# Kernel tuning notes

Measured on AMD Instinct MI355X. Metric: run time of the kernel, lower is better.

Reference implementation:

```python
import jax, jax.numpy as jnp
import numpy as np
from jax import lax

U = 45      # sliding window length (input_dim[1])
WH = 22     # half window, int(U/2)
L = 900     # fixed sequence length
D = 80      # doppler bins (input_dim[2])
DM = 40     # d_model


def _lin(x, w, b):
    return x @ w.T + b


def _conv(x, w, b):
    y = lax.conv_general_dilated(x, w, (1, 1), 'SAME', dimension_numbers=('NCHW', 'OIHW', 'NCHW'))
    return y + b[None, :, None, None]


def _pool(x, th, tw):
    return lax.reduce_window(x, -jnp.inf, lax.max, (1, 1, th, tw), (1, 1, th, tw), 'VALID')


def _encoder(x, cw1, cb1, cw2, cb2, cw3, cb3, cw4, cb4):
    x = _pool(jax.nn.elu(_conv(x, cw1, cb1)), 2, 2)  # 45x80 -> 22x40
    x = _pool(jax.nn.elu(_conv(x, cw2, cb2)), 2, 2)  # -> 11x20
    x = _pool(jax.nn.elu(_conv(x, cw3, cb3)), 2, 2)  # -> 5x10
    x = _pool(jax.nn.elu(_conv(x, cw4, cb4)), 1, 2)  # -> 5x5
    return x


def _forward(z, targets_onehot, dur, cw1, cb1, cw2, cb2, cw3, cb3, cw4, cb4,
             fc1w, fc1b, fc2w, fc2b, embw, embb, wq, bq, wk, bk, wv, bv,
             flw1, flb1, flw2, flb2, stw1, stb1, stw2, stb2, edw1, edb1, edw2, edb2):
    B = z.shape[0]
    # --- vectorized sliding-window extraction (replaces per-timestep loop) ---
    # In the original, real frames are always RIGHT-aligned inside the window
    # (zeros are concatenated at the front for both head and tail edges).
    i = jnp.arange(L)[:, None]
    j = jnp.arange(U)[None, :]
    end = jnp.minimum(i + WH + 1, L)           # exclusive end of real content
    idx = end - U + j                          # (L, U) source frame per slot
    valid = idx >= jnp.maximum(i - WH, 0)      # slots before real content are zero
    win = jnp.take(z, jnp.clip(idx, 0, L - 1), axis=2)          # (B, 1, L, U, D)
    win = jnp.where(valid[None, None, :, :, None], win, 0.0)
    win = win.transpose(0, 2, 1, 3, 4).reshape(B * L, 1, U, D)
    feat = _encoder(win, cw1, cb1, cw2, cb2, cw3, cb3, cw4, cb4).reshape(B, L, 400)
    # classifier_1 (dropout = identity in eval)
    z_p = _lin(jax.nn.elu(_lin(feat, fc1w, fc1b)), fc2w, fc2b)   # (B, L, 40)
    t = jnp.broadcast_to(targets_onehot[:, None, :], (B, L, targets_onehot.shape[-1]))
    z_t = jax.nn.elu(_lin(jnp.concatenate([z_p, t], axis=-1), embw, embb))  # (B, L, 40)
    # masked self-attention
    q = _lin(z_t, wq, bq)
    k = _lin(z_t, wk, bk)
    v = _lin(z_t, wv, bv)
    score = jnp.einsum('bld,bmd->blm', q, k) / jnp.sqrt(jnp.float32(DM))
    m = jnp.arange(L)[None, :] < dur[:, None]                    # (B, L)
    mask = m[:, :, None] & m[:, None, :]                         # (B, L, L)
    # original: score*mask then masked_fill(mask==0, -1e-12)
    score = jnp.where(mask, score, jnp.float32(-1e-12))
    attn = jax.nn.softmax(score, axis=-1)
    x = attn @ v + z_t

    def head(h, w1, b1, w2, b2):
        return _lin(jax.nn.elu(_lin(h, w1, b1)), w2, b2)[..., 0]

    fl = head(x, flw1, flb1, flw2, flb2)
    st = head(x, stw1, stb1, stw2, stb2)
    ed = head(x, edw1, edb1, edw2, edb2)
    return fl, st, ed


_PARAM_SHAPES = [('cw1', (4, 1, 3, 3)), ('cb1', (4,)), ('cw2', (8, 4, 3, 3)), ('cb2', (8,)),
                 ('cw3', (16, 8, 3, 3)), ('cb3', (16,)), ('cw4', (16, 16, 3, 3)), ('cb4', (16,)),
                 ('fc1w', (128, 400)), ('fc1b', (128,)), ('fc2w', (40, 128)), ('fc2b', (40,)),
                 ('embw', (40, 45)), ('embb', (40,)),
                 ('wq', (40, 40)), ('bq', (40,)), ('wk', (40, 40)), ('bk', (40,)), ('wv', (40, 40)), ('bv', (40,)),
                 ('flw1', (10, 40)), ('flb1', (10,)), ('flw2', (1, 10)), ('flb2', (1,)),
                 ('stw1', (10, 40)), ('stb1', (10,)), ('stw2', (1, 10)), ('stb2', (1,)),
                 ('edw1', (10, 40)), ('edb1', (10,)), ('edw2', (1, 10)), ('edb2', (1,))]


def setup_inputs() -> dict:
    key = jax.random.key(0)
    ks = jax.random.split(key, 64)
    B = 4
    inp = {}
    inp['z'] = jax.random.normal(ks[0], (B, 1, L, D), jnp.float32)
    inp['targets_onehot'] = jax.nn.one_hot(jax.random.randint(ks[1], (B,), 0, 5), 5, dtype=jnp.float32)
    inp['dur'] = jax.random.randint(ks[2], (B,), 1, L + 1)
    for t, (name, shp) in enumerate(_PARAM_SHAPES):
        inp[name] = jax.random.normal(ks[3 + t], shp, jnp.float32) * 0.05
    return inp


def reference(z, targets_onehot, dur, cw1, cb1, cw2, cb2, cw3, cb3, cw4, cb4,
              fc1w, fc1b, fc2w, fc2b, embw, embb, wq, bq, wk, bk, wv, bv,
              flw1, flb1, flw2, flb2, stw1, stb1, stw2, stb2, edw1, edb1, edw2, edb2):
    return _forward(z, targets_onehot, dur, cw1, cb1, cw2, cb2, cw3, cb3, cw4, cb4,
                    fc1w, fc1b, fc2w, fc2b, embw, embb, wq, bq, wk, bk, wv, bv,
                    flw1, flb1, flw2, flb2, stw1, stb1, stw2, stb2, edw1, edb1, edw2, edb2)
```

## Files before the change

kernel.cpp:

```cpp
#include <hip/hip_runtime.h>

typedef unsigned int u32;
typedef _Float16 f16;
typedef f16 f16x2 __attribute__((ext_vector_type(2)));
typedef f16 f16x4 __attribute__((ext_vector_type(4)));
typedef f16 f16x8 __attribute__((ext_vector_type(8)));
typedef float f32x4 __attribute__((ext_vector_type(4)));

#define LSEQ 900
#define BATCH 4
#define NWIN (BATCH*LSEQ)
#define NBLK NWIN
#define MT 57
#define NABLK (BATCH*MT)

__device__ __forceinline__ float eluf(float x){ return x > 0.f ? x : __expf(x) - 1.f; }
#define BC2(u) __builtin_bit_cast(f16x2, (u))
#define ZERO4H ((f16x4){(f16)0,(f16)0,(f16)0,(f16)0})
#define ZERO8H __builtin_bit_cast(f16x8, (uint4{0,0,0,0}))

#define P0U 0
#define P1U 2112
#define FEATU 3872
#define F32U 4080
#define SMTOT 4288
#define T1F 0
#define H2F 4224
#define T2F 0
#define H3F 4224
#define T3F 0
#define FEATF 7744

#define WB2A 0
#define WB2B 512
#define WB3  768
#define WB4  2304
#define WFC1 5376
#define WEND 58624
#define WPM  58624
#define WPTE (WPM + 576000)
#define WPZ  (WPTE + 576000)
#define WQH  (WPZ + 576000)
#define WKH  (WQH + 145920)
#define WVT  (WKH + 145920)
#define WF32 ((WVT + 145920)/2)

#define PREP_BLOCKS ((WEND+255)/256)
#define CONV_BLOCKS ((144000+255)/256)

__global__ __launch_bounds__(256) void prep_all(
    const float* __restrict__ z,
    const float* __restrict__ cw1, const float* __restrict__ cb1,
    const float* __restrict__ cw2, const float* __restrict__ cw3,
    const float* __restrict__ cw4, const float* __restrict__ fc1w,
    f16* __restrict__ wsF, f16* __restrict__ PM, f16* __restrict__ PTE, f16* __restrict__ PZ)
{
  const int blk = blockIdx.x;
  if (blk < PREP_BLOCKS) {
    const int g = blk*256 + threadIdx.x;
    if (g >= WEND) return;
    float val;
    if (g < 512) {
      const int l = g>>3, j = g&7;
      const int oc = l&15, c = l>>4;
      const int dr = c>>1, dc = 2*(c&1) + (j>>2), ic = j&3;
      val = (oc<8 && dc<3) ? cw2[oc*36 + ic*9 + dr*3 + dc] : 0.f;
    } else if (g < 768) {
      const int u = g-512, l = u>>2, j = u&3;
      const int oc = l&15, dc = l>>4, ic = j;
      val = (oc<8 && dc<3) ? cw2[oc*36 + ic*9 + 6 + dc] : 0.f;
    } else if (g < 2304) {
      const int u = g-768, dr = u>>9, r = u&511, l = r>>3, j = r&7;
      const int oc = l&15, dc = l>>4, ic = j;
      val = (dc<3) ? cw3[oc*72 + ic*9 + dr*3 + dc] : 0.f;
    } else if (g < 5376) {
      const int u = g-2304, v = u>>9, dr = v>>1, h = v&1;
      const int r = u&511, l = r>>3, j = r&7;
      const int oc = l&15, chunk = l>>4;
      const int dcl = chunk>>1, ic = (chunk&1)*8 + j, dc = h*2 + dcl;
      val = (dc<3) ? cw4[oc*144 + ic*9 + dr*3 + dc] : 0.f;
    } else {
      const int u = g - WFC1;
      const int j = u&7, l = (u>>3)&63, st = (u>>9)%13, nt = u/(13*512);
      const int k = st*32 + (l>>4)*8 + j, n = nt*16 + (l&15);
      val = (k<400) ? fc1w[n*400 + k] : 0.f;
    }
    wsF[g] = (f16)val;
  } else {
    const int g = (blk - PREP_BLOCKS)*256 + threadIdx.x;
    if (g >= 144000) return;
    const int cp = g % 40, fb2 = g / 40, f = fb2 % 900, b = fb2 / 900;
    if (f >= 899) return;
    const int c0 = 2*cp;
    const float* zb = z + b*72000;
    float p[4][4];
    #pragma unroll
    for (int dr = 0; dr < 4; ++dr) {
      const int r = f - 1 + dr;
      const bool rok = (r >= 0) && (r < 900);
      #pragma unroll
      for (int dc = 0; dc < 4; ++dc) {
        const int cc = c0 + dc - 1;
        p[dr][dc] = (rok && cc >= 0 && cc < 80) ? zb[r*80+cc] : 0.f;
      }
    }
    f16x4 opm, opte, opz;
    #pragma unroll
    for (int oc = 0; oc < 4; ++oc) {
      float pmv = -3.4e38f, ptev = -3.4e38f, pzv = -3.4e38f;
      #pragma unroll
      for (int col = 0; col < 2; ++col) {
        float te = cb1[oc];
        float s0 = 0.f;
        float c1n = cb1[oc];
        #pragma unroll
        for (int dc = 0; dc < 3; ++dc) {
          const float w0 = cw1[oc*9 + dc], w1 = cw1[oc*9 + 3 + dc], w2 = cw1[oc*9 + 6 + dc];
          s0  += w0 * p[0][col+dc];
          te  += w1 * p[1][col+dc] + w2 * p[2][col+dc];
          c1n += w0 * p[1][col+dc] + w1 * p[2][col+dc] + w2 * p[3][col+dc];
        }
        const float cf = te + s0;
        pmv  = fmaxf(pmv,  fmaxf(cf, c1n));
        ptev = fmaxf(ptev, fmaxf(te, c1n));
        pzv  = fmaxf(pzv,  fmaxf(te, 0.f));
      }
      opm[oc]  = (f16)eluf(pmv);
      opte[oc] = (f16)eluf(ptev);
      opz[oc]  = (f16)eluf(pzv);
    }
    *(f16x4*)(PM  + g*4) = opm;
    *(f16x4*)(PTE + g*4) = opte;
    *(f16x4*)(PZ  + g*4) = opz;
  }
}

__global__ __launch_bounds__(256,8) void encoder6(
    const f16* __restrict__ PM, const f16* __restrict__ PTE, const f16* __restrict__ PZ,
    const float* __restrict__ toh,
    const float* __restrict__ cb2, const float* __restrict__ cb3, const float* __restrict__ cb4,
    const f16* __restrict__ wsF,
    const float* __restrict__ fc1b, const float* __restrict__ fc2w, const float* __restrict__ fc2b,
    const float* __restrict__ embw, const float* __restrict__ embb,
    const float* __restrict__ wq, const float* __restrict__ bq,
    const float* __restrict__ wk, const float* __restrict__ bk,
    const float* __restrict__ wv, const float* __restrict__ bv,
    float* __restrict__ zt_g, f16* __restrict__ qh,
    f16* __restrict__ kh, f16* __restrict__ vT)
{
  __shared__ __align__(16) u32 sm[SMTOT];
  f16* smh = (f16*)sm;
  const int tid = threadIdx.x, blk = blockIdx.x;
  const int lane = tid & 63, wid = tid >> 6;
  const int b = blk/LSEQ, i0 = blk%LSEQ;

  {
    const int e45 = min(i0 + 23, LSEQ) - 45;
    const int sv  = max(i0 - 22, 0);
    const f16* PMb  = PM  + b*144000;
    const f16* PTEb = PTE + b*144000;
    const f16* PZb  = PZ  + b*144000;
    for (int s = tid; s < 440; s += 256) {
      const int pr = s/20, pcp = s%20;
      const int fa = e45 + 2*pr;
      f16x8 v = ZERO8H;
      if (fa > sv)         v = *(const f16x8*)(PMb  + (fa*40 + 2*pcp)*4);
      else if (fa == sv)   v = *(const f16x8*)(PTEb + (fa*40 + 2*pcp)*4);
      else if (fa == sv-1) v = *(const f16x8*)(PZb  + (sv*40 + 2*pcp)*4);
      f16* dst = smh + T1F + ((pr+1)*44 + 2*pcp+1)*4;
      *(f16x4*)(dst)     = __builtin_shufflevector(v, v, 0,1,2,3);
      *(f16x4*)(dst + 4) = __builtin_shufflevector(v, v, 4,5,6,7);
    }
    for (int s = tid; s < 176; s += 256) {
      int r, c;
      if (s < 44)      { r = 0;  c = s; }
      else if (s < 88) { r = 23; c = s-44; }
      else {
        const int t = s - 88;
        const int which = t / 22;
        r = (t % 22) + 1;
        c = which == 0 ? 0 : (which == 1 ? 41 : (which == 2 ? 42 : 43));
      }
      *(f16x4*)(smh + T1F + (r*44+c)*4) = ZERO4H;
    }
    if (tid < 2) ((uint4*)(sm))[FEATU/4 + 50 + tid] = (uint4){0,0,0,0};
  }
  __syncthreads();

  {
    const f16x8 B2a = *(const f16x8*)(wsF + WB2A + lane*8);
    const f16x4 B2b = *(const f16x4*)(wsF + WB2B + lane*4);
    const int oc = lane&15, chunk = lane>>4;
    const float bias2 = (oc<8) ? cb2[oc] : 0.f;
    int r2 = (wid*16 + oc)/40, c2 = (wid*16 + oc)%40;
    int rE = (wid*16 + chunk*4)/40, cE = (wid*16 + chunk*4)%40;
    for (int t = wid; t < 55; t += 4) {
      const f16* base = smh + T1F;
      const f16* pA = base + ((r2 + (chunk>>1))*44 + c2 + 2*(chunk&1))*4;
      const f16x4 lo = *(const f16x4*)(pA);
      const f16x4 hi = *(const f16x4*)(pA + 4);
      const f16x8 a8 = __builtin_shufflevector(lo, hi, 0,1,2,3,4,5,6,7);
      f32x4 acc = {bias2, bias2, bias2, bias2};
      acc = __builtin_amdgcn_mfma_f32_16x16x32_f16(a8, B2a, acc, 0, 0, 0);
      const f16x4 a4 = *(const f16x4*)(base + ((r2+2)*44 + c2 + chunk)*4);
      acc = __builtin_amdgcn_mfma_f32_16x16x16f16(a4, B2b, acc, 0, 0, 0);
      if (oc < 8) {
        f16* h2o = smh + H2F;
        h2o[(rE*20 + (cE>>1))*8 + oc] = (f16)fmaxf(acc[0], acc[1]);
        const int cE2 = cE + 2;
        const int rE2 = rE + (cE2 >= 40 ? 1 : 0);
        const int cE3 = cE2 >= 40 ? cE2 - 40 : cE2;
        h2o[(rE2*20 + (cE3>>1))*8 + oc] = (f16)fmaxf(acc[2], acc[3]);
      }
      { const int cn = c2 + 24; const int cy = cn >= 40;
        r2 += 1 + cy; c2 = cy ? cn - 40 : cn; }
      { const int cn = cE + 24; const int cy = cn >= 40;
        rE += 1 + cy; cE = cy ? cn - 40 : cn; }
    }
  }
  __syncthreads();

  {
    for (int s = tid; s < 312; s += 256) {
      const int r = s/24, c = s%24;
      if (!(r>=1 && r<=11 && c>=1 && c<=20)) {
        const uint4 z4 = {0,0,0,0};
        *(uint4*)(smh + T2F + (r*24+c)*8) = z4;
      }
    }
    for (int s = tid; s < 880; s += 256) {
      const int pr = s/80, rem = s%80, cp = rem/4, op = rem%4;
      const u32* h2 = (const u32*)(smh + H2F);
      const u32 a  = h2[((2*pr  )*20 + cp)*4 + op];
      const u32 b2 = h2[((2*pr+1)*20 + cp)*4 + op];
      const f16x2 av = BC2(a), bv = BC2(b2);
      f16x2 o;
      o.x = (f16)eluf(fmaxf((float)av.x, (float)bv.x));
      o.y = (f16)eluf(fmaxf((float)av.y, (float)bv.y));
      ((u32*)(smh + T2F))[((pr+1)*24 + cp+1)*4 + op] = __builtin_bit_cast(u32, o);
    }
  }
  __syncthreads();

  {
    f16x8 B3r[3];
    #pragma unroll
    for (int dr = 0; dr < 3; ++dr) B3r[dr] = *(const f16x8*)(wsF + WB3 + dr*512 + lane*8);
    const int oc = lane&15, chunk = lane>>4;
    const float bias3 = cb3[oc];
    for (int t = wid; t < 14; t += 4) {
      const int mA = t*16 + oc;
      const int r3 = mA/20, c3 = mA%20;
      const f16* base = smh + T2F;
      f32x4 acc = {bias3, bias3, bias3, bias3};
      #pragma unroll
      for (int dr = 0; dr < 3; ++dr) {
        const f16x8 a8 = *(const f16x8*)(base + ((r3+dr)*24 + c3 + chunk)*8);
        acc = __builtin_amdgcn_mfma_f32_16x16x32_f16(a8, B3r[dr], acc, 0, 0, 0);
      }
      #pragma unroll
      for (int p = 0; p < 2; ++p) {
        const int mE = t*16 + chunk*4 + 2*p;
        if (mE < 220) {
          const int rE = mE/20, cE = mE%20;
          if (rE < 10)
            smh[H3F + (rE*10 + (cE>>1))*16 + oc] = (f16)fmaxf(acc[2*p], acc[2*p+1]);
        }
      }
    }
  }
  __syncthreads();

  {
    for (int s = tid; s < 98; s += 256) {
      const int r = s/14, c = s%14;
      if (!(r>=1 && r<=5 && c>=1 && c<=10)) {
        const uint4 z4 = {0,0,0,0};
        *(uint4*)(smh + T3F + (r*14+c)*16)     = z4;
        *(uint4*)(smh + T3F + (r*14+c)*16 + 8) = z4;
      }
    }
    for (int s = tid; s < 400; s += 256) {
      const int pr = s/80, rem = s%80, cp = rem/8, op = rem%8;
      const u32* h3 = (const u32*)(smh + H3F);
      const u32 a  = h3[((2*pr  )*10 + cp)*8 + op];
      const u32 b2 = h3[((2*pr+1)*10 + cp)*8 + op];
      const f16x2 av = BC2(a), bv = BC2(b2);
      f16x2 o;
      o.x = (f16)eluf(fmaxf((float)av.x, (float)bv.x));
      o.y = (f16)eluf(fmaxf((float)av.y, (float)bv.y));
      ((u32*)(smh + T3F))[((pr+1)*14 + cp+1)*8 + op] = __builtin_bit_cast(u32, o);
    }
  }
  __syncthreads();

  {
    f16x8 B4r[6];
    #pragma unroll
    for (int v = 0; v < 6; ++v) B4r[v] = *(const f16x8*)(wsF + WB4 + v*512 + lane*8);
    const int oc = lane&15, chunk = lane>>4;
    const int dcl = chunk>>1, hsel = chunk&1;
    const float bias4 = cb4[oc];
    for (int t = wid; t < 4; t += 4) {
      const int mA = t*16 + oc;
      const int mmA = mA < 50 ? mA : mA - 50;
      const int r4 = mmA/10, c4 = mmA%10;
      const f16* base = smh + T3F;
      f32x4 acc = {bias4, bias4, bias4, bias4};
      #pragma unroll
      for (int v = 0; v < 6; ++v) {
        const int dr = v>>1, h = v&1;
        const f16x8 a8 = *(const f16x8*)(base + ((r4+dr)*14 + c4 + h*2 + dcl)*16 + hsel*8);
        acc = __builtin_amdgcn_mfma_f32_16x16x32_f16(a8, B4r[v], acc, 0, 0, 0);
      }
      #pragma unroll
      for (int p = 0; p < 2; ++p) {
        const int mE = t*16 + chunk*4 + 2*p;
        if (mE < 50) {
          const int rE = mE/10, cE = mE%10;
          smh[FEATF + oc*25 + rE*5 + (cE>>1)] = (f16)eluf(fmaxf(acc[2*p], acc[2*p+1]));
        }
      }
    }
  }
  __syncthreads();

  {
    float* h1 = (float*)(sm + F32U);
    #pragma unroll
    for (int q2 = 0; q2 < 2; ++q2) {
      const int nt = wid + q2*4;
      f32x4 acc = {0.f, 0.f, 0.f, 0.f};
      for (int st = 0; st < 13; ++st) {
        const f16x8 a8 = *(const f16x8*)(smh + FEATF + st*32 + (lane>>4)*8);
        const f16x8 b8 = *(const f16x8*)(wsF + WFC1 + ((nt*13 + st)*64 + lane)*8);
        acc = __builtin_amdgcn_mfma_f32_16x16x32_f16(a8, b8, acc, 0, 0, 0);
      }
      if (lane < 16) {
        const int n = nt*16 + lane;
        h1[n] = eluf(acc[0] + fc1b[n]);
      }
    }
  }
  __syncthreads();

  if (wid == 0) {
    float* h1f = (float*)(sm + F32U);
    float* zpf = h1f + 128;
    float* ztf = h1f + 168;
    if (lane < 40) {
      const float4* hv = (const float4*)h1f;
      const float4* wr = (const float4*)(fc2w + lane*128);
      float acc = fc2b[lane];
      #pragma unroll 8
      for (int c = 0; c < 32; ++c) {
        const float4 a = wr[c], x = hv[c];
        acc += a.x*x.x + a.y*x.y + a.z*x.z + a.w*x.w;
      }
      zpf[lane] = acc;
    }
    if (lane < 40) {
      const float* wr = embw + lane*45;
      float acc = embb[lane];
      #pragma unroll 8
      for (int j = 0; j < 40; ++j) acc += wr[j]*zpf[j];
      #pragma unroll
      for (int j = 0; j < 5; ++j)  acc += wr[40+j]*toh[b*5 + j];
      const float v2 = eluf(acc);
      ztf[lane] = v2;
      zt_g[(b*LSEQ + i0)*40 + lane] = v2;
    }
    if (lane < 40) {
      const float4* zv = (const float4*)ztf;
      float4 zr[10];
      #pragma unroll
      for (int c = 0; c < 10; ++c) zr[c] = zv[c];
      float res[3];
      #pragma unroll
      for (int which = 0; which < 3; ++which) {
        const float* wm = which==0 ? wq : (which==1 ? wk : wv);
        const float* bb = which==0 ? bq : (which==1 ? bk : bv);
        const float4* wr = (const float4*)(wm + lane*40);
        float acc = bb[lane];
        #pragma unroll
        for (int c = 0; c < 10; ++c) {
          const float4 a = wr[c], x = zr[c];
          acc += a.x*x.x + a.y*x.y + a.z*x.z + a.w*x.w;
        }
        res[which] = acc;
      }
      qh[b*36480 + i0*40 + lane] = (f16)res[0];
      kh[b*36480 + i0*40 + lane] = (f16)res[1];
      vT[b*36480 + lane*912 + i0] = (f16)res[2];
    }
  }
}

__global__ __launch_bounds__(512) void attn7(
    const f16* __restrict__ qh, const f16* __restrict__ kh,
    const f16* __restrict__ vT, const float* __restrict__ zt_g,
    const int* __restrict__ dur,
    const float* __restrict__ flw1, const float* __restrict__ flb1,
    const float* __restrict__ flw2, const float* __restrict__ flb2,
    const float* __restrict__ stw1, const float* __restrict__ stb1,
    const float* __restrict__ stw2, const float* __restrict__ stb2,
    const float* __restrict__ edw1, const float* __restrict__ edb1,
    const float* __restrict__ edw2, const float* __restrict__ edb2,
    float* __restrict__ out)
{
  __shared__ __align__(16) f16 P[16*916];
  __shared__ float denp[8][16];
  __shared__ float pvp[8][16][48];
  __shared__ __align__(16) float xr[16][40];
  __shared__ float hb[16][30];

  const int tid = threadIdx.x;
  const int w = tid >> 6, l = tid & 63;
  const int col = l & 15, kg = l >> 4;
  const int blk = blockIdx.x;
  const int b = blk / MT, mt = blk % MT;
  const int m0 = mt * 16;
  const int durb = dur[b];
  const float scale = 0.15811388300841897f;

  const f16* qb = qh + b*36480;
  const f16* kb = kh + b*36480;
  const f16* vb = vT + b*36480;

  f16x4 aq[3];
  #pragma unroll
  for (int kst = 0; kst < 3; ++kst) {
    const int k0 = kst*16 + kg*4;
    aq[kst] = (k0 < 40) ? *(const f16x4*)(qb + (m0 + col)*40 + k0) : ZERO4H;
  }

  float sum4[4] = {0.f, 0.f, 0.f, 0.f};
  for (int nt = w; nt < 57; nt += 8) {
    const int n = nt*16 + col;
    f32x4 acc = {0.f, 0.f, 0.f, 0.f};
    #pragma unroll
    for (int kst = 0; kst < 3; ++kst) {
      const int k0 = kst*16 + kg*4;
      const f16x4 bfrag = (k0 < 40) ? *(const f16x4*)(kb + n*40 + k0) : ZERO4H;
      acc = __builtin_amdgcn_mfma_f32_16x16x16f16(aq[kst], bfrag, acc, 0, 0, 0);
    }
    #pragma unroll
    for (int i = 0; i < 4; ++i) {
      const int mrow = kg*4 + i;
      const int mg = m0 + mrow;
      float p;
      if (n >= 900)                    p = 0.f;
      else if (mg >= durb || n >= durb) p = 1.f;
      else                              p = __expf(acc[i]*scale);
      P[mrow*916 + n] = (f16)p;
      sum4[i] += p;
    }
  }
  #pragma unroll
  for (int i = 0; i < 4; ++i) {
    #pragma unroll
    for (int off = 1; off < 16; off <<= 1) sum4[i] += __shfl_xor(sum4[i], off);
  }
  if (col == 0) {
    #pragma unroll
    for (int i = 0; i < 4; ++i) denp[w][kg*4 + i] = sum4[i];
  }
  __syncthreads();

  {
    f32x4 acc3[3] = {{0.f,0.f,0.f,0.f},{0.f,0.f,0.f,0.f},{0.f,0.f,0.f,0.f}};
    for (int kt = w; kt < 57; kt += 8) {
      const f16x4 ap = *(const f16x4*)(P + col*916 + kt*16 + kg*4);
      #pragma unroll
      for (int nt = 0; nt < 3; ++nt) {
        const int n = nt*16 + col;
        const f16x4 bv = (n < 40) ? *(const f16x4*)(vb + n*912 + kt*16 + kg*4) : ZERO4H;
        acc3[nt] = __builtin_amdgcn_mfma_f32_16x16x16f16(ap, bv, acc3[nt], 0, 0, 0);
      }
    }
    #pragma unroll
    for (int nt = 0; nt < 3; ++nt)
      #pragma unroll
      for (int i = 0; i < 4; ++i)
        pvp[w][kg*4 + i][nt*16 + col] = acc3[nt][i];
  }
  __syncthreads();

  for (int s = tid; s < 640; s += 512) {
    const int m = s/40, d = s%40;
    float den = 0.f, pv = 0.f;
    #pragma unroll
    for (int ww = 0; ww < 8; ++ww) { den += denp[ww][m]; pv += pvp[ww][m][d]; }
    const int mg = min(m0 + m, 899);
    xr[m][d] = pv/den + zt_g[(b*LSEQ + mg)*40 + d];
  }
  __syncthreads();

  if (tid < 480) {
    const int m = tid/30, rr = tid%30, hd = rr/10, j = rr%10;
    const float* w1 = hd==0?flw1:(hd==1?stw1:edw1);
    const float* b1 = hd==0?flb1:(hd==1?stb1:edb1);
    float a = b1[j];
    #pragma unroll 8
    for (int d = 0; d < 40; ++d) a += w1[j*40+d]*xr[m][d];
    hb[m][hd*10+j] = eluf(a);
  }
  __syncthreads();
  if (tid < 48) {
    const int m = tid/3, hd = tid%3;
    if (m0 + m < 900) {
      const float* w2 = hd==0?flw2:(hd==1?stw2:edw2);
      const float* b2 = hd==0?flb2:(hd==1?stb2:edb2);
      float a = b2[0];
      #pragma unroll
      for (int j = 0; j < 10; ++j) a += w2[j]*hb[m][hd*10+j];
      out[hd*NWIN + b*LSEQ + m0 + m] = a;
    }
  }
}

extern "C" void kernel_launch(void* const* d_in, const int* in_sizes, int n_in,
                              void* d_out, int out_size, void* d_ws, size_t ws_size,
                              hipStream_t stream) {
  const float* z    = (const float*)d_in[0];
  const float* toh  = (const float*)d_in[1];
  const int*   dur  = (const int*)d_in[2];
  const float* cw1  = (const float*)d_in[3];
  const float* cb1  = (const float*)d_in[4];
  const float* cw2  = (const float*)d_in[5];
  const float* cb2  = (const float*)d_in[6];
  const float* cw3  = (const float*)d_in[7];
  const float* cb3  = (const float*)d_in[8];
  const float* cw4  = (const float*)d_in[9];
  const float* cb4  = (const float*)d_in[10];
  const float* fc1w = (const float*)d_in[11];
  const float* fc1b = (const float*)d_in[12];
  const float* fc2w = (const float*)d_in[13];
  const float* fc2b = (const float*)d_in[14];
  const float* embw = (const float*)d_in[15];
  const float* embb = (const float*)d_in[16];
  const float* wq   = (const float*)d_in[17];
  const float* bq   = (const float*)d_in[18];
  const float* wk   = (const float*)d_in[19];
  const float* bk   = (const float*)d_in[20];
  const float* wv   = (const float*)d_in[21];
  const float* bv   = (const float*)d_in[22];
  const float* flw1 = (const float*)d_in[23];
  const float* flb1 = (const float*)d_in[24];
  const float* flw2 = (const float*)d_in[25];
  const float* flb2 = (const float*)d_in[26];
  const float* stw1 = (const float*)d_in[27];
  const float* stb1 = (const float*)d_in[28];
  const float* stw2 = (const float*)d_in[29];
  const float* stb2 = (const float*)d_in[30];
  const float* edw1 = (const float*)d_in[31];
  const float* edb1 = (const float*)d_in[32];
  const float* edw2 = (const float*)d_in[33];
  const float* edb2 = (const float*)d_in[34];

  f16*   wsF = (f16*)d_ws;
  f16*   PM  = wsF + WPM;
  f16*   PTE = wsF + WPTE;
  f16*   PZ  = wsF + WPZ;
  f16*   qh  = wsF + WQH;
  f16*   kh  = wsF + WKH;
  f16*   vT  = wsF + WVT;
  float* zt  = (float*)d_ws + WF32;

  prep_all<<<PREP_BLOCKS + CONV_BLOCKS, 256, 0, stream>>>(z, cw1, cb1, cw2, cw3, cw4, fc1w,
                                                          wsF, PM, PTE, PZ);
  encoder6<<<NBLK, 256, 0, stream>>>(PM, PTE, PZ, toh, cb2, cb3, cb4, wsF,
                                     fc1b, fc2w, fc2b, embw, embb,
                                     wq, bq, wk, bk, wv, bv, zt, qh, kh, vT);
  attn7<<<NABLK, 512, 0, stream>>>(qh, kh, vT, zt, dur,
                                   flw1, flb1, flw2, flb2,
                                   stw1, stb1, stw2, stb2,
                                   edw1, edb1, edw2, edb2,
                                   (float*)d_out);
}
```

Baseline: 70.26 us.

## Split encoder tail into separate batched head/QKV kernel over 8 rows

Moves the fc2, embedding and Q/K/V projections out of the per-window encoder block, where only one wavefront did this serial work after a barrier, into a new kernel that processes 8 rows per block using all 256 threads. The encoder now writes the fc1 hidden activations to global memory. This is meant to remove the idle single-wave tail from each encoder block and cut its shared-memory use. In exchange it adds a kernel launch and a global round trip for the 128-float hidden vector per row.

```diff
diff --git a/kernel.cpp b/kernel.cpp
--- a/kernel.cpp
+++ b/kernel.cpp
@@ -13,6 +13,7 @@
 #define NBLK NWIN
 #define MT 57
 #define NABLK (BATCH*MT)
+#define NHBLK (NWIN/8)
 
 __device__ __forceinline__ float eluf(float x){ return x > 0.f ? x : __expf(x) - 1.f; }
 #define BC2(u) __builtin_bit_cast(f16x2, (u))
@@ -22,8 +23,7 @@
 #define P0U 0
 #define P1U 2112
 #define FEATU 3872
-#define F32U 4080
-#define SMTOT 4288
+#define SMTOT 4080
 #define T1F 0
 #define H2F 4224
 #define T2F 0
@@ -135,18 +135,11 @@
   }
 }
 
-__global__ __launch_bounds__(256,8) void encoder6(
+__global__ __launch_bounds__(256,8) void encoder7(
     const f16* __restrict__ PM, const f16* __restrict__ PTE, const f16* __restrict__ PZ,
-    const float* __restrict__ toh,
     const float* __restrict__ cb2, const float* __restrict__ cb3, const float* __restrict__ cb4,
-    const f16* __restrict__ wsF,
-    const float* __restrict__ fc1b, const float* __restrict__ fc2w, const float* __restrict__ fc2b,
-    const float* __restrict__ embw, const float* __restrict__ embb,
-    const float* __restrict__ wq, const float* __restrict__ bq,
-    const float* __restrict__ wk, const float* __restrict__ bk,
-    const float* __restrict__ wv, const float* __restrict__ bv,
-    float* __restrict__ zt_g, f16* __restrict__ qh,
-    f16* __restrict__ kh, f16* __restrict__ vT)
+    const f16* __restrict__ wsF, const float* __restrict__ fc1b,
+    float* __restrict__ h1g)
 {
   __shared__ __align__(16) u32 sm[SMTOT];
   f16* smh = (f16*)sm;
@@ -326,7 +319,7 @@
   __syncthreads();
 
   {
-    float* h1 = (float*)(sm + F32U);
+    float* dst = h1g + (b*LSEQ + i0)*128;
     #pragma unroll
     for (int q2 = 0; q2 < 2; ++q2) {
       const int nt = wid + q2*4;
@@ -338,61 +331,79 @@
       }
       if (lane < 16) {
         const int n = nt*16 + lane;
-        h1[n] = eluf(acc[0] + fc1b[n]);
-      }
-    }
-  }
-  __syncthreads();
-
-  if (wid == 0) {
-    float* h1f = (float*)(sm + F32U);
-    float* zpf = h1f + 128;
-    float* ztf = h1f + 168;
-    if (lane < 40) {
-      const float4* hv = (const float4*)h1f;
-      const float4* wr = (const float4*)(fc2w + lane*128);
-      float acc = fc2b[lane];
-      #pragma unroll 8
-      for (int c = 0; c < 32; ++c) {
-        const float4 a = wr[c], x = hv[c];
-        acc += a.x*x.x + a.y*x.y + a.z*x.z + a.w*x.w;
-      }
-      zpf[lane] = acc;
-    }
-    if (lane < 40) {
-      const float* wr = embw + lane*45;
-      float acc = embb[lane];
-      #pragma unroll 8
-      for (int j = 0; j < 40; ++j) acc += wr[j]*zpf[j];
-      #pragma unroll
-      for (int j = 0; j < 5; ++j)  acc += wr[40+j]*toh[b*5 + j];
-      const float v2 = eluf(acc);
-      ztf[lane] = v2;
-      zt_g[(b*LSEQ + i0)*40 + lane] = v2;
-    }
-    if (lane < 40) {
-      const float4* zv = (const float4*)ztf;
-      float4 zr[10];
-      #pragma unroll
-      for (int c = 0; c < 10; ++c) zr[c] = zv[c];
-      float res[3];
-      #pragma unroll
-      for (int which = 0; which < 3; ++which) {
-        const float* wm = which==0 ? wq : (which==1 ? wk : wv);
-        const float* bb = which==0 ? bq : (which==1 ? bk : bv);
-        const float4* wr = (const float4*)(wm + lane*40);
-        float acc = bb[lane];
-        #pragma unroll
-        for (int c = 0; c < 10; ++c) {
-          const float4 a = wr[c], x = zr[c];
-          acc += a.x*x.x + a.y*x.y + a.z*x.z + a.w*x.w;
-        }
-        res[which] = acc;
-      }
-      qh[b*36480 + i0*40 + lane] = (f16)res[0];
-      kh[b*36480 + i0*40 + lane] = (f16)res[1];
-      vT[b*36480 + lane*912 + i0] = (f16)res[2];
-    }
+        dst[n] = eluf(acc[0] + fc1b[n]);
+      }
+    }
+  }
+}
+
+__global__ __launch_bounds__(256) void head_qkv(
+    const float* __restrict__ h1g, const float* __restrict__ toh,
+    const float* __restrict__ fc2w, const float* __restrict__ fc2b,
+    const float* __restrict__ embw, const float* __restrict__ embb,
+    const float* __restrict__ wq, const float* __restrict__ bq,
+    const float* __restrict__ wk, const float* __restrict__ bk,
+    const float* __restrict__ wv, const float* __restrict__ bv,
+    float* __restrict__ zt_g, f16* __restrict__ qh,
+    f16* __restrict__ kh, f16* __restrict__ vT)
+{
+  __shared__ __align__(16) float h1s[8][128];
+  __shared__ __align__(16) float zps[8][40];
+  __shared__ __align__(16) float zts[8][40];
+  const int tid = threadIdx.x, blk = blockIdx.x;
+  const int r0 = blk*8;
+
+  {
+    const int r = tid >> 5, c = tid & 31;
+    ((float4*)h1s[r])[c] = ((const float4*)(h1g + (r0+r)*128))[c];
+  }
+  __syncthreads();
+
+  for (int s = tid; s < 320; s += 256) {
+    const int r = s/40, n = s%40;
+    const float4* hv = (const float4*)h1s[r];
+    const float4* wr = (const float4*)(fc2w + n*128);
+    float acc = fc2b[n];
+    #pragma unroll 8
+    for (int c = 0; c < 32; ++c) {
+      const float4 a = wr[c], x = hv[c];
+      acc += a.x*x.x + a.y*x.y + a.z*x.z + a.w*x.w;
+    }
+    zps[r][n] = acc;
+  }
+  __syncthreads();
+
+  for (int s = tid; s < 320; s += 256) {
+    const int r = s/40, n = s%40;
+    const int row = r0 + r, b = row/LSEQ;
+    const float* wr = embw + n*45;
+    float acc = embb[n];
+    #pragma unroll 8
+    for (int j = 0; j < 40; ++j) acc += wr[j]*zps[r][j];
+    #pragma unroll
+    for (int j = 0; j < 5; ++j)  acc += wr[40+j]*toh[b*5 + j];
+    const float v = eluf(acc);
+    zts[r][n] = v;
+    zt_g[row*40 + n] = v;
+  }
+  __syncthreads();
+
+  for (int s = tid; s < 960; s += 256) {
+    const int which = s/320, u = s%320, r = u/40, n = u%40;
+    const int row = r0 + r, b = row/LSEQ, i = row%LSEQ;
+    const float* wm = which==0 ? wq : (which==1 ? wk : wv);
+    const float* bb = which==0 ? bq : (which==1 ? bk : bv);
+    const float4* wr = (const float4*)(wm + n*40);
+    const float4* zv = (const float4*)zts[r];
+    float acc = bb[n];
+    #pragma unroll
+    for (int c = 0; c < 10; ++c) {
+      const float4 a = wr[c], x = zv[c];
+      acc += a.x*x.x + a.y*x.y + a.z*x.z + a.w*x.w;
+    }
+    if (which == 0)      qh[b*36480 + i*40 + n] = (f16)acc;
+    else if (which == 1) kh[b*36480 + i*40 + n] = (f16)acc;
+    else                 vT[b*36480 + n*912 + i] = (f16)acc;
   }
 }
 
@@ -566,12 +577,13 @@
   f16*   kh  = wsF + WKH;
   f16*   vT  = wsF + WVT;
   float* zt  = (float*)d_ws + WF32;
+  float* h1g = (float*)d_ws + WF32 + 144000;
 
   prep_all<<<PREP_BLOCKS + CONV_BLOCKS, 256, 0, stream>>>(z, cw1, cb1, cw2, cw3, cw4, fc1w,
                                                           wsF, PM, PTE, PZ);
-  encoder6<<<NBLK, 256, 0, stream>>>(PM, PTE, PZ, toh, cb2, cb3, cb4, wsF,
-                                     fc1b, fc2w, fc2b, embw, embb,
-                                     wq, bq, wk, bk, wv, bv, zt, qh, kh, vT);
+  encoder7<<<NBLK, 256, 0, stream>>>(PM, PTE, PZ, cb2, cb3, cb4, wsF, fc1b, h1g);
+  head_qkv<<<NHBLK, 256, 0, stream>>>(h1g, toh, fc2w, fc2b, embw, embb,
+                                      wq, bq, wk, bk, wv, bv, zt, qh, kh, vT);
   attn7<<<NABLK, 512, 0, stream>>>(qh, kh, vT, zt, dur,
                                    flw1, flb1, flw2, flb2,
                                    stw1, stb1, stw2, stb2,
```

New measurement: 76.16 us. 1.08x slower.
